# Performance work log

Measured on AMD Instinct MI355X. Metric: run time of the kernel, lower is better.

The kernel has to match this reference:

```python
import jax, jax.numpy as jnp
import numpy as np

N = 20000      # total nodes (heterogeneous node types flattened)
N1 = 6000      # first node-type slice for decoder z1
N2 = 6000      # second node-type slice for decoder z2
R = 3          # relations
E = 200000     # edges per relation
HID = 128      # hidden_dim (input feature dim for gat_1)
NDIM = 64      # noise dim
D1 = 64        # hidden_dim1 (per-head out feats of gat_1/gat_e)
D2 = 32        # hidden_dim2 = zdim
H1 = 4         # num_heads
H2 = 2         # num_heads // 2
S = 2          # K + J noise copies
REWEIGHT = ((NDIM + D1) / (HID + D1)) ** 0.5


def _rgat(x, W, al, ar, src, dst, act):
    """Multi-relation GAT layer: per-relation gather -> edge softmax -> scatter, summed over relations, mean over heads.
    x: [N, Din]; W: [R, Din, H*F]; al/ar: [R, H, F]; src/dst: [R, E] int."""
    Rr, H, F = al.shape
    out = jnp.zeros((N, H, F), x.dtype)
    for r in range(Rr):  # small fixed relation loop (structurally distinct weights)
        h = (x @ W[r]).reshape(N, H, F)               # [N,H,F]
        el = jnp.sum(h * al[r][None], axis=-1)        # [N,H]
        er = jnp.sum(h * ar[r][None], axis=-1)        # [N,H]
        s_, d_ = src[r], dst[r]
        e = jax.nn.leaky_relu(el[s_] + er[d_], 0.2)   # [E,H]
        m = jax.ops.segment_max(e, d_, num_segments=N)
        m = jnp.where(jnp.isfinite(m), m, jnp.zeros_like(m))
        w = jnp.exp(e - m[d_])
        denom = jax.ops.segment_sum(w, d_, num_segments=N)
        alpha = w / (denom[d_] + 1e-16)               # edge softmax per dst
        out = out + jax.ops.segment_sum(alpha[:, :, None] * h[s_], d_, num_segments=N)
    return act(jnp.mean(out, axis=1))                 # mean over heads -> [N,F]


def setup_inputs() -> dict:
    key = jax.random.key(0)
    ks = jax.random.split(key, 20)
    d = {}
    d['x'] = jax.random.normal(ks[0], (N, HID), jnp.float32)
    # Bernoulli(0.5) noise scaled by reweight, as in node_encode
    d['noise'] = (jax.random.uniform(ks[1], (S, N, NDIM)) < 0.5).astype(jnp.float32) * REWEIGHT
    sc = 0.1
    d['W1'] = sc * jax.random.normal(ks[2], (R, HID, H1 * D1), jnp.float32)
    d['al1'] = sc * jax.random.normal(ks[3], (R, H1, D1), jnp.float32)
    d['ar1'] = sc * jax.random.normal(ks[4], (R, H1, D1), jnp.float32)
    d['We'] = sc * jax.random.normal(ks[5], (R, NDIM, H1 * D1), jnp.float32)
    d['ale'] = sc * jax.random.normal(ks[6], (R, H1, D1), jnp.float32)
    d['are'] = sc * jax.random.normal(ks[7], (R, H1, D1), jnp.float32)
    d['W2'] = sc * jax.random.normal(ks[8], (R, D1, H2 * D2), jnp.float32)
    d['al2'] = sc * jax.random.normal(ks[9], (R, H2, D2), jnp.float32)
    d['ar2'] = sc * jax.random.normal(ks[10], (R, H2, D2), jnp.float32)
    d['W3'] = sc * jax.random.normal(ks[11], (R, D1, H2 * D2), jnp.float32)
    d['al3'] = sc * jax.random.normal(ks[12], (R, H2, D2), jnp.float32)
    d['ar3'] = sc * jax.random.normal(ks[13], (R, H2, D2), jnp.float32)
    d['rk_lgt'] = jax.random.uniform(ks[14], (1, D2), jnp.float32, -6.0, 0.0)
    d['src'] = jax.random.randint(ks[15], (R, E), 0, N, jnp.int32)
    d['dst'] = jax.random.randint(ks[16], (R, E), 0, N, jnp.int32)
    return d


def reference(x, noise, W1, al1, ar1, We, ale, are, W2, al2, ar2, W3, al3, ar3, rk_lgt, src, dst):
    relu = jax.nn.relu
    ident = lambda v: v
    # hiddenx = gat_1(x); hiddene = gat_e(noise) per sample; hidden1 = hiddenx + hiddene
    hiddenx = _rgat(x, W1, al1, ar1, src, dst, relu)                                  # [N,D1]
    hiddene = jax.vmap(lambda nz: _rgat(nz, We, ale, are, src, dst, relu))(noise)     # [S,N,D1]
    hidden1 = hiddenx[None] + hiddene                                                 # [S,N,D1]
    # mu = gat_2(hidden1); encsto='semi' -> logvar = gat_3(hiddenx)
    mu = jax.vmap(lambda h: _rgat(h, W2, al2, ar2, src, dst, ident))(hidden1)         # [S,N,D2]
    logvar = _rgat(hiddenx, W3, al3, ar3, src, dst, ident)                            # [N,D2]
    # GraphDecoder (eval mode: dropout off, z = mu): bmm inner-product + sigmoid
    rk2 = jax.nn.sigmoid(rk_lgt)                                                      # rk.pow(2)
    z1 = mu[:, :N1]                                                                   # [S,N1,D2]
    z2 = mu[:, N1:N1 + N2]                                                            # [S,N2,D2]
    adj = jax.nn.sigmoid(jnp.einsum('sid,sjd->sij', z1, z2))                          # [S,N1,N2]
    adj = jnp.mean(adj, axis=0, keepdims=True)                                        # eval: mean over samples
    return (adj, mu, logvar, rk2)
```

## Files before the change

### kernel.cpp

```cpp
#include <hip/hip_runtime.h>
#include <hip/hip_bf16.h>


static constexpr int N_  = 20000;
static constexpr int R_  = 3;
static constexpr int E_  = 200000;
static constexpr int NB1 = 6000;

__device__ __forceinline__ float sigmoidf_(float x) {
  return 1.0f / (1.0f + __expf(-x));
}

__global__ void hist_kernel(const int* __restrict__ dst, int* __restrict__ counts) {
  int i = blockIdx.x * blockDim.x + threadIdx.x;
  if (i >= R_ * E_) return;
  int r = i / E_;
  atomicAdd(&counts[r * N_ + dst[i]], 1);
}

__global__ void scan_kernel(const int* __restrict__ counts, int* __restrict__ ptr) {
  int r = blockIdx.x;
  __shared__ int buf[1024];
  __shared__ int carry;
  int tid = threadIdx.x;
  if (tid == 0) carry = 0;
  __syncthreads();
  for (int base = 0; base < N_; base += 1024) {
    int i = base + tid;
    int v = (i < N_) ? counts[r * N_ + i] : 0;
    buf[tid] = v;
    __syncthreads();
    for (int off = 1; off < 1024; off <<= 1) {
      int t = (tid >= off) ? buf[tid - off] : 0;
      __syncthreads();
      buf[tid] += t;
      __syncthreads();
    }
    int c = carry;
    if (i < N_) ptr[r * (N_ + 1) + i] = c + buf[tid] - v;
    __syncthreads();
    if (tid == 1023) carry = c + buf[1023];
    __syncthreads();
  }
  if (tid == 0) ptr[r * (N_ + 1) + N_] = carry;
}

__global__ void scatter_kernel(const int* __restrict__ src, const int* __restrict__ dst,
                               const int* __restrict__ ptr, int* __restrict__ fill,
                               int* __restrict__ csrc) {
  int i = blockIdx.x * blockDim.x + threadIdx.x;
  if (i >= R_ * E_) return;
  int r = i / E_;
  int d = dst[i];
  int pos = ptr[r * (N_ + 1) + d] + atomicAdd(&fill[r * N_ + d], 1);
  csrc[r * E_ + pos] = src[i];
}

template <int DIN, int HF, int H, int F>
__global__ __launch_bounds__(256) void gemm_el_kernel(
    const float* __restrict__ A, const float* __restrict__ W,
    const float* __restrict__ al, const float* __restrict__ ar,
    float* __restrict__ h, float* __restrict__ el, float* __restrict__ er) {
  __shared__ float sAT[64][68];
  __shared__ float sW[64][68];
  const int nb  = blockIdx.x * 64;
  const int cg  = blockIdx.y;
  const int r   = blockIdx.z;
  const int tid = threadIdx.x;
  const int ty  = tid >> 4, tx = tid & 15;

  float acc[4][4];
#pragma unroll
  for (int i = 0; i < 4; ++i)
#pragma unroll
    for (int j = 0; j < 4; ++j) acc[i][j] = 0.f;

  for (int k0 = 0; k0 < DIN; k0 += 64) {
    for (int idx = tid; idx < 4096; idx += 256) {
      int nl = idx >> 6, kk = idx & 63;
      int n = nb + nl;
      sAT[kk][nl] = (n < N_) ? A[(size_t)n * DIN + k0 + kk] : 0.f;
    }
    for (int idx = tid; idx < 4096; idx += 256) {
      int kk = idx >> 6, cl = idx & 63;
      sW[kk][cl] = W[((size_t)r * DIN + k0 + kk) * HF + cg * 64 + cl];
    }
    __syncthreads();
#pragma unroll 8
    for (int kk = 0; kk < 64; ++kk) {
      const float4 a4 = *(const float4*)&sAT[kk][ty * 4];
      const float4 w4 = *(const float4*)&sW[kk][tx * 4];
      const float a[4] = {a4.x, a4.y, a4.z, a4.w};
      const float w[4] = {w4.x, w4.y, w4.z, w4.w};
#pragma unroll
      for (int i = 0; i < 4; ++i)
#pragma unroll
        for (int j = 0; j < 4; ++j) acc[i][j] = fmaf(a[i], w[j], acc[i][j]);
    }
    __syncthreads();
  }

  const int c0 = cg * 64 + tx * 4;
#pragma unroll
  for (int i = 0; i < 4; ++i) {
    int n = nb + ty * 4 + i;
    if (n < N_) {
      float4 v; v.x = acc[i][0]; v.y = acc[i][1]; v.z = acc[i][2]; v.w = acc[i][3];
      *(float4*)&h[((size_t)r * N_ + n) * HF + c0] = v;
    }
  }

  const int hh = c0 / F;
  const int f0 = c0 % F;
  float al4[4], ar4[4];
#pragma unroll
  for (int j = 0; j < 4; ++j) {
    al4[j] = al[((size_t)r * H + hh) * F + f0 + j];
    ar4[j] = ar[((size_t)r * H + hh) * F + f0 + j];
  }
  float elp[4], erp[4];
#pragma unroll
  for (int i = 0; i < 4; ++i) {
    elp[i] = acc[i][0] * al4[0] + acc[i][1] * al4[1] + acc[i][2] * al4[2] + acc[i][3] * al4[3];
    erp[i] = acc[i][0] * ar4[0] + acc[i][1] * ar4[1] + acc[i][2] * ar4[2] + acc[i][3] * ar4[3];
  }
  constexpr int G = F / 4;
#pragma unroll
  for (int off = G / 2; off >= 1; off >>= 1) {
#pragma unroll
    for (int i = 0; i < 4; ++i) {
      elp[i] += __shfl_down(elp[i], off, G);
      erp[i] += __shfl_down(erp[i], off, G);
    }
  }
  if ((tx & (G - 1)) == 0) {
#pragma unroll
    for (int i = 0; i < 4; ++i) {
      int n = nb + ty * 4 + i;
      if (n < N_) {
        el[((size_t)r * N_ + n) * H + hh] = elp[i];
        er[((size_t)r * N_ + n) * H + hh] = erp[i];
      }
    }
  }
}

template <int H, int F, bool RELU>
__global__ __launch_bounds__(256) void agg_kernel(
    const float* __restrict__ h, const float* __restrict__ el, const float* __restrict__ er,
    const int* __restrict__ ptr, const int* __restrict__ srcs,
    const float* __restrict__ base, float* __restrict__ outf) {
  constexpr int VL  = F / 4;
  constexpr int EPG = 64 / VL;
  const int n    = blockIdx.x;
  const int wave = threadIdx.x >> 6;
  const int lane = threadIdx.x & 63;
  const int eg   = lane / VL;
  const int fl   = lane % VL;

  float4 tot = {0.f, 0.f, 0.f, 0.f};

  for (int r = 0; r < R_; ++r) {
    const int p0  = ptr[r * (N_ + 1) + n];
    const int deg = ptr[r * (N_ + 1) + n + 1] - p0;
    if (deg == 0) continue;
    const int* sp = srcs + (size_t)r * E_ + p0;
    const float erv = er[((size_t)r * N_ + n) * H + wave];

    float m = -3.0e38f, dsum = 0.f;
    float4 racc = {0.f, 0.f, 0.f, 0.f};

    for (int b0 = 0; b0 < deg; b0 += 64) {
      const int cnt = min(64, deg - b0);
      int   s = 0;
      float e = -3.0e38f;
      if (lane < cnt) {
        s = sp[b0 + lane];
        e = el[((size_t)r * N_ + s) * H + wave] + erv;
        e = (e > 0.f) ? e : 0.2f * e;
      }
      float mloc = e;
#pragma unroll
      for (int off = 32; off >= 1; off >>= 1)
        mloc = fmaxf(mloc, __shfl_xor(mloc, off, 64));
      const float mnew  = fmaxf(m, mloc);
      const float scale = __expf(m - mnew);
      const float w = __expf(e - mnew);
      float wsum = w;
#pragma unroll
      for (int off = 32; off >= 1; off >>= 1)
        wsum += __shfl_xor(wsum, off, 64);
      dsum = fmaf(dsum, scale, wsum);
      racc.x *= scale; racc.y *= scale; racc.z *= scale; racc.w *= scale;
      m = mnew;

      const int kmax = (cnt + EPG - 1) / EPG;
      for (int k = 0; k < kmax; ++k) {
        const int i2 = eg + k * EPG;
        const int   s2 = __shfl(s, i2, 64);
        const float w2 = __shfl(w, i2, 64);
        const float4 hv =
            *(const float4*)&h[((size_t)r * N_ + s2) * (H * F) + wave * F + fl * 4];
        racc.x = fmaf(w2, hv.x, racc.x);
        racc.y = fmaf(w2, hv.y, racc.y);
        racc.z = fmaf(w2, hv.z, racc.z);
        racc.w = fmaf(w2, hv.w, racc.w);
      }
    }
    const float inv = 1.0f / (dsum + 1e-16f);
    tot.x = fmaf(racc.x, inv, tot.x);
    tot.y = fmaf(racc.y, inv, tot.y);
    tot.z = fmaf(racc.z, inv, tot.z);
    tot.w = fmaf(racc.w, inv, tot.w);
  }

#pragma unroll
  for (int off = VL; off < 64; off <<= 1) {
    tot.x += __shfl_xor(tot.x, off, 64);
    tot.y += __shfl_xor(tot.y, off, 64);
    tot.z += __shfl_xor(tot.z, off, 64);
    tot.w += __shfl_xor(tot.w, off, 64);
  }

  __shared__ float4 sh4[H][VL];
  if (eg == 0) sh4[wave][fl] = tot;
  __syncthreads();
  if (threadIdx.x < VL) {
    float4 v = sh4[0][threadIdx.x];
#pragma unroll
    for (int hh = 1; hh < H; ++hh) {
      float4 u = sh4[hh][threadIdx.x];
      v.x += u.x; v.y += u.y; v.z += u.z; v.w += u.w;
    }
    const float sc = 1.0f / H;
    v.x *= sc; v.y *= sc; v.z *= sc; v.w *= sc;
    if (RELU) {
      v.x = fmaxf(v.x, 0.f); v.y = fmaxf(v.y, 0.f);
      v.z = fmaxf(v.z, 0.f); v.w = fmaxf(v.w, 0.f);
    }
    if (base) {
      float4 bv = *(const float4*)&base[(size_t)n * F + threadIdx.x * 4];
      v.x += bv.x; v.y += bv.y; v.z += bv.z; v.w += bv.w;
    }
    *(float4*)&outf[(size_t)n * F + threadIdx.x * 4] = v;
  }
}

__global__ __launch_bounds__(512) void adj_kernel(const float* __restrict__ mu,
                                                  float* __restrict__ out) {
  __shared__ float sA[32][128];
  __shared__ float sB[32][128];
  const int jb = blockIdx.x * 128;
  const int ib = blockIdx.y * 128;
  const int tid = threadIdx.x;
  const int ty = tid >> 5;
  const int tx = tid & 31;

  float res[8][4];
#pragma unroll
  for (int i = 0; i < 8; ++i)
#pragma unroll
    for (int j = 0; j < 4; ++j) res[i][j] = 0.f;

  for (int s = 0; s < 2; ++s) {
    __syncthreads();
#pragma unroll
    for (int it = 0; it < 2; ++it) {
      int idx = tid + it * 512;
      int dg = idx >> 7, row = idx & 127;
      int gi = ib + row;
      int gj = jb + row;
      float4 va = {0.f, 0.f, 0.f, 0.f}, vb = {0.f, 0.f, 0.f, 0.f};
      if (gi < NB1) va = *(const float4*)&mu[((size_t)s * N_ + gi) * 32 + dg * 4];
      if (gj < NB1) vb = *(const float4*)&mu[((size_t)s * N_ + NB1 + gj) * 32 + dg * 4];
      sA[dg * 4 + 0][row] = va.x; sA[dg * 4 + 1][row] = va.y;
      sA[dg * 4 + 2][row] = va.z; sA[dg * 4 + 3][row] = va.w;
      sB[dg * 4 + 0][row] = vb.x; sB[dg * 4 + 1][row] = vb.y;
      sB[dg * 4 + 2][row] = vb.z; sB[dg * 4 + 3][row] = vb.w;
    }
    __syncthreads();

    float acc[8][4];
#pragma unroll
    for (int i = 0; i < 8; ++i)
#pragma unroll
      for (int j = 0; j < 4; ++j) acc[i][j] = 0.f;
#pragma unroll 8
    for (int k = 0; k < 32; ++k) {
      float a[8], b[4];
      *(float4*)&a[0] = *(const float4*)&sA[k][ty * 4];
      *(float4*)&a[4] = *(const float4*)&sA[k][64 + ty * 4];
      *(float4*)&b[0] = *(const float4*)&sB[k][tx * 4];
#pragma unroll
      for (int i = 0; i < 8; ++i)
#pragma unroll
        for (int j = 0; j < 4; ++j) acc[i][j] = fmaf(a[i], b[j], acc[i][j]);
    }
#pragma unroll
    for (int i = 0; i < 8; ++i)
#pragma unroll
      for (int j = 0; j < 4; ++j) res[i][j] += sigmoidf_(acc[i][j]);
  }

  const bool fullc = (jb + 128) <= NB1;
#pragma unroll
  for (int i = 0; i < 8; ++i) {
    int row = ib + ((i < 4) ? (ty * 4 + i) : (64 + ty * 4 + (i - 4)));
    if (row < NB1) {
      int col = jb + tx * 4;
      if (fullc) {
        float4 p;
        p.x = 0.5f * res[i][0]; p.y = 0.5f * res[i][1];
        p.z = 0.5f * res[i][2]; p.w = 0.5f * res[i][3];
        *(float4*)&out[(size_t)row * NB1 + col] = p;
      } else {
#pragma unroll
        for (int j = 0; j < 4; ++j) {
          if (col + j < NB1) out[(size_t)row * NB1 + col + j] = 0.5f * res[i][j];
        }
      }
    }
  }
}

__global__ void rk2_kernel(const float* __restrict__ rk_lgt, float* __restrict__ out) {
  int i = threadIdx.x;
  if (i < 32) out[i] = sigmoidf_(rk_lgt[i]);
}

static inline size_t align256(size_t x) { return (x + 255) & ~(size_t)255; }

extern "C" void kernel_launch(void* const* d_in, const int* in_sizes, int n_in,
                              void* d_out, int out_size, void* d_ws, size_t ws_size,
                              hipStream_t stream) {
  (void)in_sizes; (void)n_in; (void)out_size; (void)d_ws; (void)ws_size;
  const float* x      = (const float*)d_in[0];
  const float* noise  = (const float*)d_in[1];
  const float* W1     = (const float*)d_in[2];
  const float* al1    = (const float*)d_in[3];
  const float* ar1    = (const float*)d_in[4];
  const float* We     = (const float*)d_in[5];
  const float* ale    = (const float*)d_in[6];
  const float* are    = (const float*)d_in[7];
  const float* W2     = (const float*)d_in[8];
  const float* al2    = (const float*)d_in[9];
  const float* ar2    = (const float*)d_in[10];
  const float* W3     = (const float*)d_in[11];
  const float* al3    = (const float*)d_in[12];
  const float* ar3    = (const float*)d_in[13];
  const float* rk_lgt = (const float*)d_in[14];
  const int*   src    = (const int*)d_in[15];
  const int*   dst    = (const int*)d_in[16];

  float* out_adj    = (float*)d_out;
  float* out_mu     = out_adj + (size_t)NB1 * NB1;
  float* out_logvar = out_mu + (size_t)2 * N_ * 32;
  float* out_rk2    = out_logvar + (size_t)N_ * 32;

  char* sc = (char*)d_out;
  size_t off = 0;
  int*   ptr     = (int*)(sc + off);   off += align256((size_t)R_ * (N_ + 1) * 4);
  int*   csr_src = (int*)(sc + off);   off += align256((size_t)R_ * E_ * 4);
  float* el      = (float*)(sc + off); off += align256((size_t)R_ * N_ * 4 * 4);
  float* er      = (float*)(sc + off); off += align256((size_t)R_ * N_ * 4 * 4);
  float* hx      = (float*)(sc + off); off += align256((size_t)N_ * 64 * 4);
  float* h1      = (float*)(sc + off); off += align256((size_t)2 * N_ * 64 * 4);
  float* h       = (float*)(sc + off); off += align256((size_t)R_ * N_ * 256 * 4);
  int* counts = (int*)(void*)h;
  int* fill   = (int*)(void*)((char*)(void*)h + align256((size_t)R_ * N_ * 4));

  hipMemsetAsync(counts, 0, (size_t)R_ * N_ * 4, stream);
  hipMemsetAsync(fill, 0, (size_t)R_ * N_ * 4, stream);
  int eblocks = (R_ * E_ + 255) / 256;
  hist_kernel<<<eblocks, 256, 0, stream>>>(dst, counts);
  scan_kernel<<<R_, 1024, 0, stream>>>(counts, ptr);
  scatter_kernel<<<eblocks, 256, 0, stream>>>(src, dst, ptr, fill, csr_src);

  const dim3 g256((N_ + 63) / 64, 4, R_);
  const dim3 g64((N_ + 63) / 64, 1, R_);

  gemm_el_kernel<128, 256, 4, 64><<<g256, 256, 0, stream>>>(x, W1, al1, ar1, h, el, er);
  agg_kernel<4, 64, true><<<N_, 256, 0, stream>>>(h, el, er, ptr, csr_src, nullptr, hx);

  for (int s = 0; s < 2; ++s) {
    gemm_el_kernel<64, 256, 4, 64><<<g256, 256, 0, stream>>>(
        noise + (size_t)s * N_ * 64, We, ale, are, h, el, er);
    agg_kernel<4, 64, true><<<N_, 256, 0, stream>>>(
        h, el, er, ptr, csr_src, hx, h1 + (size_t)s * N_ * 64);
  }

  for (int s = 0; s < 2; ++s) {
    gemm_el_kernel<64, 64, 2, 32><<<g64, 256, 0, stream>>>(
        h1 + (size_t)s * N_ * 64, W2, al2, ar2, h, el, er);
    agg_kernel<2, 32, false><<<N_, 128, 0, stream>>>(
        h, el, er, ptr, csr_src, nullptr, out_mu + (size_t)s * N_ * 32);
  }

  gemm_el_kernel<64, 64, 2, 32><<<g64, 256, 0, stream>>>(hx, W3, al3, ar3, h, el, er);
  agg_kernel<2, 32, false><<<N_, 128, 0, stream>>>(
      h, el, er, ptr, csr_src, nullptr, out_logvar);

  rk2_kernel<<<1, 32, 0, stream>>>(rk_lgt, out_rk2);

  adj_kernel<<<dim3((NB1 + 127) / 128, (NB1 + 127) / 128), 512, 0, stream>>>(out_mu, out_adj);
}
```

Measured before the change: 1.027 ms.

## Parallelize CSR scan across chunks and batch the three second-layer GAT passes

Result: faster. 971.1 us (-5.4%).

```diff
diff --git a/kernel.cpp b/kernel.cpp
--- a/kernel.cpp
+++ b/kernel.cpp
@@ -18,31 +18,45 @@
   atomicAdd(&counts[r * N_ + dst[i]], 1);
 }
 
-__global__ void scan_kernel(const int* __restrict__ counts, int* __restrict__ ptr) {
-  int r = blockIdx.x;
-  __shared__ int buf[1024];
-  __shared__ int carry;
-  int tid = threadIdx.x;
-  if (tid == 0) carry = 0;
+static constexpr int SCAN_CH = 1024;
+static constexpr int NCH = (N_ + SCAN_CH - 1) / SCAN_CH;
+
+__global__ __launch_bounds__(1024) void scan_partial_kernel(
+    const int* __restrict__ counts, int* __restrict__ ptr, int* __restrict__ csums) {
+  const int r = blockIdx.y, c = blockIdx.x, tid = threadIdx.x;
+  __shared__ int buf[SCAN_CH];
+  const int i = c * SCAN_CH + tid;
+  const int v = (i < N_) ? counts[r * N_ + i] : 0;
+  buf[tid] = v;
   __syncthreads();
-  for (int base = 0; base < N_; base += 1024) {
-    int i = base + tid;
-    int v = (i < N_) ? counts[r * N_ + i] : 0;
-    buf[tid] = v;
-    __syncthreads();
-    for (int off = 1; off < 1024; off <<= 1) {
-      int t = (tid >= off) ? buf[tid - off] : 0;
-      __syncthreads();
-      buf[tid] += t;
-      __syncthreads();
-    }
-    int c = carry;
-    if (i < N_) ptr[r * (N_ + 1) + i] = c + buf[tid] - v;
-    __syncthreads();
-    if (tid == 1023) carry = c + buf[1023];
-    __syncthreads();
-  }
-  if (tid == 0) ptr[r * (N_ + 1) + N_] = carry;
+  for (int off = 1; off < SCAN_CH; off <<= 1) {
+    int t = (tid >= off) ? buf[tid - off] : 0;
+    __syncthreads();
+    buf[tid] += t;
+    __syncthreads();
+  }
+  if (i < N_) ptr[r * (N_ + 1) + i] = buf[tid] - v;
+  if (tid == SCAN_CH - 1) csums[r * NCH + c] = buf[tid];
+}
+
+__global__ void scan_sums_kernel(int* __restrict__ csums, int* __restrict__ ptr) {
+  int r = threadIdx.x;
+  if (r < R_) {
+    int acc = 0;
+    for (int c = 0; c < NCH; ++c) {
+      int t = csums[r * NCH + c];
+      csums[r * NCH + c] = acc;
+      acc += t;
+    }
+    ptr[r * (N_ + 1) + N_] = acc;
+  }
+}
+
+__global__ __launch_bounds__(1024) void scan_add_kernel(
+    const int* __restrict__ csums, int* __restrict__ ptr) {
+  const int r = blockIdx.y, c = blockIdx.x, tid = threadIdx.x;
+  const int i = c * SCAN_CH + tid;
+  if (i < N_) ptr[r * (N_ + 1) + i] += csums[r * NCH + c];
 }
 
 __global__ void scatter_kernel(const int* __restrict__ src, const int* __restrict__ dst,
@@ -57,15 +71,14 @@
 }
 
 template <int DIN, int HF, int H, int F>
-__global__ __launch_bounds__(256) void gemm_el_kernel(
-    const float* __restrict__ A, const float* __restrict__ W,
+__device__ __forceinline__ void gemm_el_dev(
+    const int r, const float* __restrict__ A, const float* __restrict__ W,
     const float* __restrict__ al, const float* __restrict__ ar,
     float* __restrict__ h, float* __restrict__ el, float* __restrict__ er) {
   __shared__ float sAT[64][68];
   __shared__ float sW[64][68];
   const int nb  = blockIdx.x * 64;
   const int cg  = blockIdx.y;
-  const int r   = blockIdx.z;
   const int tid = threadIdx.x;
   const int ty  = tid >> 4, tx = tid & 15;
 
@@ -145,14 +158,34 @@
   }
 }
 
+template <int DIN, int HF, int H, int F>
+__global__ __launch_bounds__(256) void gemm_el_kernel(
+    const float* __restrict__ A, const float* __restrict__ W,
+    const float* __restrict__ al, const float* __restrict__ ar,
+    float* __restrict__ h, float* __restrict__ el, float* __restrict__ er) {
+  gemm_el_dev<DIN, HF, H, F>(blockIdx.z, A, W, al, ar, h, el, er);
+}
+
+struct GemmB3 {
+  const float* A[3]; const float* W[3]; const float* al[3]; const float* ar[3];
+  float* h[3]; float* el[3]; float* er[3];
+};
+template <int DIN, int HF, int H, int F>
+__global__ __launch_bounds__(256) void gemm_el_b3_kernel(GemmB3 a) {
+  const int inst = blockIdx.z / R_;
+  const int r    = blockIdx.z % R_;
+  gemm_el_dev<DIN, HF, H, F>(r, a.A[inst], a.W[inst], a.al[inst], a.ar[inst],
+                             a.h[inst], a.el[inst], a.er[inst]);
+}
+
 template <int H, int F, bool RELU>
-__global__ __launch_bounds__(256) void agg_kernel(
-    const float* __restrict__ h, const float* __restrict__ el, const float* __restrict__ er,
-    const int* __restrict__ ptr, const int* __restrict__ srcs,
-    const float* __restrict__ base, float* __restrict__ outf) {
+__device__ __forceinline__ void agg_dev(
+    const int n, const float* __restrict__ h, const float* __restrict__ el,
+    const float* __restrict__ er, const int* __restrict__ ptr,
+    const int* __restrict__ srcs, const float* __restrict__ base,
+    float* __restrict__ outf) {
   constexpr int VL  = F / 4;
   constexpr int EPG = 64 / VL;
-  const int n    = blockIdx.x;
   const int wave = threadIdx.x >> 6;
   const int lane = threadIdx.x & 63;
   const int eg   = lane / VL;
@@ -244,6 +277,24 @@
     }
     *(float4*)&outf[(size_t)n * F + threadIdx.x * 4] = v;
   }
+}
+
+template <int H, int F, bool RELU>
+__global__ __launch_bounds__(256) void agg_kernel(
+    const float* __restrict__ h, const float* __restrict__ el, const float* __restrict__ er,
+    const int* __restrict__ ptr, const int* __restrict__ srcs,
+    const float* __restrict__ base, float* __restrict__ outf) {
+  agg_dev<H, F, RELU>(blockIdx.x, h, el, er, ptr, srcs, base, outf);
+}
+
+struct AggB3 {
+  const float* h[3]; const float* el[3]; const float* er[3]; float* out[3];
+};
+__global__ __launch_bounds__(128) void agg_b3_kernel(
+    AggB3 a, const int* __restrict__ ptr, const int* __restrict__ srcs) {
+  const int inst = blockIdx.y;
+  agg_dev<2, 32, false>(blockIdx.x, a.h[inst], a.el[inst], a.er[inst],
+                        ptr, srcs, nullptr, a.out[inst]);
 }
 
 __global__ __launch_bounds__(512) void adj_kernel(const float* __restrict__ mu,
@@ -360,24 +411,29 @@
   char* sc = (char*)d_out;
   size_t off = 0;
   int*   ptr     = (int*)(sc + off);   off += align256((size_t)R_ * (N_ + 1) * 4);
+  int*   csums   = (int*)(sc + off);   off += align256((size_t)R_ * NCH * 4);
   int*   csr_src = (int*)(sc + off);   off += align256((size_t)R_ * E_ * 4);
   float* el      = (float*)(sc + off); off += align256((size_t)R_ * N_ * 4 * 4);
   float* er      = (float*)(sc + off); off += align256((size_t)R_ * N_ * 4 * 4);
+  float* el3     = (float*)(sc + off); off += align256((size_t)3 * R_ * N_ * 2 * 4);
+  float* er3     = (float*)(sc + off); off += align256((size_t)3 * R_ * N_ * 2 * 4);
   float* hx      = (float*)(sc + off); off += align256((size_t)N_ * 64 * 4);
   float* h1      = (float*)(sc + off); off += align256((size_t)2 * N_ * 64 * 4);
   float* h       = (float*)(sc + off); off += align256((size_t)R_ * N_ * 256 * 4);
   int* counts = (int*)(void*)h;
   int* fill   = (int*)(void*)((char*)(void*)h + align256((size_t)R_ * N_ * 4));
+  float* hM3 = h;
 
   hipMemsetAsync(counts, 0, (size_t)R_ * N_ * 4, stream);
   hipMemsetAsync(fill, 0, (size_t)R_ * N_ * 4, stream);
   int eblocks = (R_ * E_ + 255) / 256;
   hist_kernel<<<eblocks, 256, 0, stream>>>(dst, counts);
-  scan_kernel<<<R_, 1024, 0, stream>>>(counts, ptr);
+  scan_partial_kernel<<<dim3(NCH, R_), SCAN_CH, 0, stream>>>(counts, ptr, csums);
+  scan_sums_kernel<<<1, 64, 0, stream>>>(csums, ptr);
+  scan_add_kernel<<<dim3(NCH, R_), SCAN_CH, 0, stream>>>(csums, ptr);
   scatter_kernel<<<eblocks, 256, 0, stream>>>(src, dst, ptr, fill, csr_src);
 
   const dim3 g256((N_ + 63) / 64, 4, R_);
-  const dim3 g64((N_ + 63) / 64, 1, R_);
 
   gemm_el_kernel<128, 256, 4, 64><<<g256, 256, 0, stream>>>(x, W1, al1, ar1, h, el, er);
   agg_kernel<4, 64, true><<<N_, 256, 0, stream>>>(h, el, er, ptr, csr_src, nullptr, hx);
@@ -389,16 +445,25 @@
         h, el, er, ptr, csr_src, hx, h1 + (size_t)s * N_ * 64);
   }
 
-  for (int s = 0; s < 2; ++s) {
-    gemm_el_kernel<64, 64, 2, 32><<<g64, 256, 0, stream>>>(
-        h1 + (size_t)s * N_ * 64, W2, al2, ar2, h, el, er);
-    agg_kernel<2, 32, false><<<N_, 128, 0, stream>>>(
-        h, el, er, ptr, csr_src, nullptr, out_mu + (size_t)s * N_ * 32);
-  }
-
-  gemm_el_kernel<64, 64, 2, 32><<<g64, 256, 0, stream>>>(hx, W3, al3, ar3, h, el, er);
-  agg_kernel<2, 32, false><<<N_, 128, 0, stream>>>(
-      h, el, er, ptr, csr_src, nullptr, out_logvar);
+  GemmB3 ga;
+  AggB3  aa;
+  const float* As[3]  = {h1, h1 + (size_t)N_ * 64, hx};
+  const float* Ws[3]  = {W2, W2, W3};
+  const float* als[3] = {al2, al2, al3};
+  const float* ars[3] = {ar2, ar2, ar3};
+  float* outs[3] = {out_mu, out_mu + (size_t)N_ * 32, out_logvar};
+  for (int i = 0; i < 3; ++i) {
+    ga.A[i]  = As[i];  ga.W[i]  = Ws[i]; ga.al[i] = als[i]; ga.ar[i] = ars[i];
+    ga.h[i]  = hM3 + (size_t)i * R_ * N_ * 64;
+    ga.el[i] = el3 + (size_t)i * R_ * N_ * 2;
+    ga.er[i] = er3 + (size_t)i * R_ * N_ * 2;
+    aa.h[i]  = ga.h[i];
+    aa.el[i] = ga.el[i];
+    aa.er[i] = ga.er[i];
+    aa.out[i] = outs[i];
+  }
+  gemm_el_b3_kernel<64, 64, 2, 32><<<dim3((N_ + 63) / 64, 1, 3 * R_), 256, 0, stream>>>(ga);
+  agg_b3_kernel<<<dim3(N_, 3), 128, 0, stream>>>(aa, ptr, csr_src);
 
   rk2_kernel<<<1, 32, 0, stream>>>(rk_lgt, out_rk2);
 
```
